# Optimization experiments

Hardware: AMD Instinct MI355X
Metric: run time of the kernel (lower is better)

## Reference

```python
import jax, jax.numpy as jnp
import numpy as np

TAKE = 64
HID = 64


def setup_inputs() -> dict:
    key = jax.random.key(0)
    ks = jax.random.split(key, 12)
    B, N, C = 32, 1000, 1601
    s = 1.0 / np.sqrt(C)
    s2 = 1.0 / np.sqrt(HID)
    return {
        "class_logits": jax.random.normal(ks[0], (B, N, C), dtype=jnp.float32),
        "proposals": jax.random.uniform(ks[1], (B, N, 4), dtype=jnp.float32),
        # subject projection (Linear stored as [in, out] so y = x @ W + b)
        "Ws1": jax.random.uniform(ks[2], (C, HID), minval=-s, maxval=s),
        "bs1": jax.random.uniform(ks[3], (HID,), minval=-s, maxval=s),
        "Ws2": jax.random.uniform(ks[4], (HID, HID), minval=-s2, maxval=s2),
        "bs2": jax.random.uniform(ks[5], (HID,), minval=-s2, maxval=s2),
        # object projection
        "Wo1": jax.random.uniform(ks[6], (C, HID), minval=-s, maxval=s),
        "bo1": jax.random.uniform(ks[7], (HID,), minval=-s, maxval=s),
        "Wo2": jax.random.uniform(ks[8], (HID, HID), minval=-s2, maxval=s2),
        "bo2": jax.random.uniform(ks[9], (HID,), minval=-s2, maxval=s2),
    }


def _mlp(x, W1, b1, W2, b2):
    # Linear -> ReLU -> Linear
    return jnp.maximum(x @ W1 + b1, 0.0) @ W2 + b2


def reference(class_logits, proposals, Ws1, bs1, Ws2, bs2, Wo1, bo1, Wo2, bo2):
    B, N, _ = class_logits.shape
    subj = _mlp(class_logits, Ws1, bs1, Ws2, bs2)  # [B, N, 64]
    obj = _mlp(class_logits, Wo1, bo1, Wo2, bo2)   # [B, N, 64]
    # relatedness[b, i, j] = sigmoid(<subj_i, obj_j>)
    scores = jax.nn.sigmoid(jnp.einsum("bnd,bmd->bnm", subj, obj))  # [B, N, N]
    flat = scores.reshape(B, N * N)
    top_scores, top_idx = jax.lax.top_k(flat, TAKE)  # descending, same as sort[:take]
    # flat index k = subject*N + object (row-major), matching the torch meshgrid
    pairs = jnp.stack([top_idx // N, top_idx % N], axis=-1)  # [B, 64, 2] (subj, obj)
    return pairs, top_scores
```

## Files before the change

kernel.cpp:

```cpp
#include <hip/hip_runtime.h>
#include <cstdint>

#define NB 32
#define NN 1000
#define NC 1601
#define HID 64
#define ROWS (NB*NN)
#define CAPB 15360
#define SROWS 15
#define NBIN 4096
#define KCH 32
#define XSTR 68
#define SSTR 132

__device__ __forceinline__ uint32_t f2key(float f){
  uint32_t u = __float_as_uint(f);
  return (u & 0x80000000u) ? ~u : (u | 0x80000000u);
}
__device__ __forceinline__ float key2f(uint32_t k){
  uint32_t u = (k & 0x80000000u) ? (k & 0x7fffffffu) : ~k;
  return __uint_as_float(u);
}

__global__ __launch_bounds__(256, 4) void mlp_kernel(
    const float* __restrict__ x,
    const float* __restrict__ Ws1, const float* __restrict__ bs1,
    const float* __restrict__ Ws2, const float* __restrict__ bs2,
    const float* __restrict__ Wo1, const float* __restrict__ bo1,
    const float* __restrict__ Wo2, const float* __restrict__ bo2,
    float* __restrict__ subj, float* __restrict__ obj)
{
  __shared__ float smem[2*KCH*XSTR];
  __shared__ float xtail[64];
  const int tid = threadIdx.x;
  const int tx  = tid & 15;
  const int ty  = tid >> 4;
  const int row0 = blockIdx.x * 64;

  float accS[4][4], accO[4][4];
  #pragma unroll
  for (int r=0;r<4;r++)
    #pragma unroll
    for (int c=0;c<4;c++){ accS[r][c]=0.f; accO[r][c]=0.f; }

  float stg[8];
  #pragma unroll
  for (int it=0; it<8; it++){
    int u = tid + it*256;
    stg[it] = x[(size_t)(row0 + (u>>5))*NC + (u&31)];
  }

  const int NCHUNK = 50;
  for (int c = 0; c < NCHUNK; c++){
    float* xT = smem + (c & 1)*(KCH*XSTR);
    #pragma unroll
    for (int it=0; it<8; it++){
      int u = tid + it*256;
      xT[(u&31)*XSTR + (u>>5)] = stg[it];
    }
    __syncthreads();
    if (c+1 < NCHUNK){
      const int k0n = (c+1)*KCH;
      #pragma unroll
      for (int it=0; it<8; it++){
        int u = tid + it*256;
        stg[it] = x[(size_t)(row0 + (u>>5))*NC + k0n + (u&31)];
      }
    }
    const float* wS = Ws1 + (size_t)(c*KCH)*HID + tx*4;
    const float* wO = Wo1 + (size_t)(c*KCH)*HID + tx*4;
    #pragma unroll 4
    for (int k=0; k<KCH; k++){
      float4 a  = *(const float4*)&xT[k*XSTR + ty*4];
      float4 bS = *(const float4*)(wS + k*HID);
      float4 bO = *(const float4*)(wO + k*HID);
      float av[4] = {a.x,a.y,a.z,a.w};
      float bs[4] = {bS.x,bS.y,bS.z,bS.w};
      float bo[4] = {bO.x,bO.y,bO.z,bO.w};
      #pragma unroll
      for (int r=0;r<4;r++)
        #pragma unroll
        for (int c2=0;c2<4;c2++){
          accS[r][c2] = fmaf(av[r], bs[c2], accS[r][c2]);
          accO[r][c2] = fmaf(av[r], bo[c2], accO[r][c2]);
        }
    }
  }

  if (tid < 64) xtail[tid] = x[(size_t)(row0 + tid)*NC + 1600];
  __syncthreads();
  {
    float4 a  = *(const float4*)&xtail[ty*4];
    float4 bS = *(const float4*)(Ws1 + (size_t)1600*HID + tx*4);
    float4 bO = *(const float4*)(Wo1 + (size_t)1600*HID + tx*4);
    float av[4] = {a.x,a.y,a.z,a.w};
    float bs[4] = {bS.x,bS.y,bS.z,bS.w};
    float bo[4] = {bO.x,bO.y,bO.z,bO.w};
    #pragma unroll
    for (int r=0;r<4;r++)
      #pragma unroll
      for (int c2=0;c2<4;c2++){
        accS[r][c2] = fmaf(av[r], bs[c2], accS[r][c2]);
        accO[r][c2] = fmaf(av[r], bo[c2], accO[r][c2]);
      }
  }

  float* hT = smem;
  #pragma unroll 1
  for (int head = 0; head < 2; head++){
    const float* b1 = head ? bo1 : bs1;
    const float* b2 = head ? bo2 : bs2;
    const float* W2 = head ? Wo2 : Ws2;
    float* yout     = head ? obj : subj;
    __syncthreads();
    #pragma unroll
    for (int jj=0; jj<4; jj++){
      float bias = b1[tx*4 + jj];
      float4 hv;
      hv.x = fmaxf((head ? accO[0][jj] : accS[0][jj]) + bias, 0.f);
      hv.y = fmaxf((head ? accO[1][jj] : accS[1][jj]) + bias, 0.f);
      hv.z = fmaxf((head ? accO[2][jj] : accS[2][jj]) + bias, 0.f);
      hv.w = fmaxf((head ? accO[3][jj] : accS[3][jj]) + bias, 0.f);
      *(float4*)&hT[(tx*4+jj)*XSTR + ty*4] = hv;
    }
    __syncthreads();
    float accY[4][4];
    #pragma unroll
    for (int c2=0;c2<4;c2++){
      float bv = b2[tx*4 + c2];
      #pragma unroll
      for (int r=0;r<4;r++) accY[r][c2] = bv;
    }
    #pragma unroll 4
    for (int d=0; d<64; d++){
      float4 a = *(const float4*)&hT[d*XSTR + ty*4];
      float4 w = *(const float4*)(W2 + d*HID + tx*4);
      float av[4] = {a.x,a.y,a.z,a.w};
      float wv[4] = {w.x,w.y,w.z,w.w};
      #pragma unroll
      for (int r=0;r<4;r++)
        #pragma unroll
        for (int c2=0;c2<4;c2++)
          accY[r][c2] = fmaf(av[r], wv[c2], accY[r][c2]);
    }
    #pragma unroll
    for (int r=0;r<4;r++)
      *(float4*)&yout[(size_t)(row0 + ty*4 + r)*HID + tx*4] =
        make_float4(accY[r][0], accY[r][1], accY[r][2], accY[r][3]);
  }
}

__global__ __launch_bounds__(256, 1) void sample_thresh(
    const float* __restrict__ subj, const float* __restrict__ obj,
    uint32_t* __restrict__ L)
{
  __shared__ float sRows[SROWS*HID];
  __shared__ uint32_t keys[SROWS*NN];
  __shared__ uint32_t hist[256];
  __shared__ uint32_t sb[2];
  const int b = blockIdx.x, tid = threadIdx.x;

  const float4* sp = (const float4*)(subj + (size_t)b*NN*HID);
  if (tid < SROWS*16) ((float4*)sRows)[tid] = sp[tid];
  __syncthreads();

  for (int j = tid; j < NN; j += 256){
    const float4* op4 = (const float4*)(obj + ((size_t)b*NN + j)*HID);
    float4 o[16];
    #pragma unroll
    for (int q=0;q<16;q++) o[q] = op4[q];
    #pragma unroll 1
    for (int i=0;i<SROWS;i++){
      const float4* s4 = (const float4*)(sRows + i*HID);
      float acc = 0.f;
      #pragma unroll
      for (int q=0;q<16;q++){
        float4 s = s4[q];
        acc = fmaf(s.x, o[q].x, acc); acc = fmaf(s.y, o[q].y, acc);
        acc = fmaf(s.z, o[q].z, acc); acc = fmaf(s.w, o[q].w, acc);
      }
      keys[i*NN + j] = f2key(acc);
    }
  }
  __syncthreads();

  uint32_t prefix = 0; int remaining = 64;
  for (int round = 0; round < 2; round++){
    const int shift = 24 - round*8;
    hist[tid] = 0;
    __syncthreads();
    for (int idx = tid; idx < SROWS*NN; idx += 256){
      uint32_t k = keys[idx];
      bool match = (round == 0) || ((k >> 24) == (prefix >> 24));
      if (match) atomicAdd(&hist[(k >> shift) & 255u], 1u);
    }
    __syncthreads();
    if (tid == 0){
      uint32_t cum = 0; int bin = 255;
      for (;; bin--){ cum += hist[bin]; if (cum >= (uint32_t)remaining || bin == 0) break; }
      sb[0] = (uint32_t)bin;
      sb[1] = (uint32_t)(remaining - (int)(cum - hist[bin]));
    }
    __syncthreads();
    prefix |= sb[0] << shift;
    remaining = (int)sb[1];
    __syncthreads();
  }
  if (tid == 0) L[b] = prefix;
}

__device__ __forceinline__ void score_tile_acc(
    const float* __restrict__ subj, const float* __restrict__ obj,
    int b, int ti, int tj, int tid,
    float* __restrict__ sT, float* __restrict__ oT, float (&acc)[8][8])
{
  const int tx = tid & 15, ty = tid >> 4;
  #pragma unroll
  for (int a=0;a<8;a++)
    #pragma unroll
    for (int c=0;c<8;c++) acc[a][c] = 0.f;

  #pragma unroll 1
  for (int half = 0; half < 2; half++){
    __syncthreads();
    {
      const float4* gp = (const float4*)subj;
      #pragma unroll
      for (int it=0; it<4; it++){
        int u = tid + it*256;
        int r = u >> 3, q = (u & 7) + half*8;
        int gr = b*NN + ti + r; gr = gr < ROWS ? gr : (ROWS-1);
        float4 v = gp[(size_t)gr*16 + q];
        int kk = (u & 7)*4;
        sT[(kk+0)*SSTR + r] = v.x;
        sT[(kk+1)*SSTR + r] = v.y;
        sT[(kk+2)*SSTR + r] = v.z;
        sT[(kk+3)*SSTR + r] = v.w;
      }
      const float4* gp2 = (const float4*)obj;
      #pragma unroll
      for (int it=0; it<4; it++){
        int u = tid + it*256;
        int r = u >> 3, q = (u & 7) + half*8;
        int gr = b*NN + tj + r; gr = gr < ROWS ? gr : (ROWS-1);
        float4 v = gp2[(size_t)gr*16 + q];
        int kk = (u & 7)*4;
        oT[(kk+0)*SSTR + r] = v.x;
        oT[(kk+1)*SSTR + r] = v.y;
        oT[(kk+2)*SSTR + r] = v.z;
        oT[(kk+3)*SSTR + r] = v.w;
      }
    }
    __syncthreads();
    #pragma unroll 2
    for (int k=0; k<32; k++){
      float4 s0 = *(const float4*)&sT[k*SSTR + ty*8];
      float4 s1 = *(const float4*)&sT[k*SSTR + ty*8 + 4];
      float4 o0 = *(const float4*)&oT[k*SSTR + tx*8];
      float4 o1 = *(const float4*)&oT[k*SSTR + tx*8 + 4];
      float s[8] = {s0.x,s0.y,s0.z,s0.w,s1.x,s1.y,s1.z,s1.w};
      float o[8] = {o0.x,o0.y,o0.z,o0.w,o1.x,o1.y,o1.z,o1.w};
      #pragma unroll
      for (int a=0;a<8;a++)
        #pragma unroll
        for (int c=0;c<8;c++)
          acc[a][c] = fmaf(s[a], o[c], acc[a][c]);
    }
  }
}

__global__ __launch_bounds__(256, 3) void score_pass1(
    const float* __restrict__ subj, const float* __restrict__ obj,
    const uint32_t* __restrict__ L, uint32_t* __restrict__ cnt,
    uint2* __restrict__ cand, uint32_t* __restrict__ ghist)
{
  __shared__ float sT[32*SSTR];
  __shared__ float oT[32*SSTR];
  __shared__ uint32_t hist[NBIN];
  __shared__ uint32_t lcnt, gbase;
  const int blk = blockIdx.x;
  const int b   = blk >> 6;
  const int t   = blk & 63;
  const int ti  = (t >> 3) << 7;
  const int tj  = (t & 7)  << 7;
  const int tid = threadIdx.x;
  const int tx = tid & 15, ty = tid >> 4;

  for (int i = tid; i < NBIN; i += 256) hist[i] = 0;
  if (tid == 0) lcnt = 0;

  float acc[8][8];
  score_tile_acc(subj, obj, b, ti, tj, tid, sT, oT, acc);

  const uint32_t Lb = L[b];
  int myCnt = 0;
  #pragma unroll
  for (int a=0;a<8;a++){
    int gi = ti + ty*8 + a;
    #pragma unroll
    for (int c=0;c<8;c++){
      int gj = tj + tx*8 + c;
      if (gi < NN && gj < NN){
        uint32_t key = f2key(acc[a][c]);
        if (key >= Lb){ myCnt++; atomicAdd(&hist[key >> 20], 1u); }
      }
    }
  }
  uint32_t lbase = atomicAdd(&lcnt, (uint32_t)myCnt);
  __syncthreads();
  if (tid == 0) gbase = atomicAdd(&cnt[b], lcnt);
  __syncthreads();
  uint32_t pos = gbase + lbase;
  #pragma unroll
  for (int a=0;a<8;a++){
    int gi = ti + ty*8 + a;
    #pragma unroll
    for (int c=0;c<8;c++){
      int gj = tj + tx*8 + c;
      if (gi < NN && gj < NN){
        uint32_t key = f2key(acc[a][c]);
        if (key >= Lb){
          if (pos < CAPB) cand[(size_t)b*CAPB + pos] = make_uint2(key, (uint32_t)(gi*NN + gj));
          pos++;
        }
      }
    }
  }
  __syncthreads();
  for (int i = tid; i < NBIN; i += 256){
    uint32_t v = hist[i];
    if (v) atomicAdd(&ghist[(size_t)b*NBIN + i], v);
  }
}

__global__ __launch_bounds__(256, 1) void pick_thresh(
    const uint32_t* __restrict__ ghist, const uint32_t* __restrict__ cnt,
    uint32_t* __restrict__ T, uint32_t* __restrict__ flag)
{
  __shared__ uint32_t S[256];
  const int b = blockIdx.x, tid = threadIdx.x;
  const uint32_t* h = ghist + (size_t)b*NBIN;
  uint32_t loc[16];
  uint32_t s = 0;
  #pragma unroll
  for (int i=0;i<16;i++){ loc[i] = h[tid*16 + i]; s += loc[i]; }
  S[tid] = s;
  __syncthreads();
  for (int off = 1; off < 256; off <<= 1){
    uint32_t v = (tid + off < 256) ? S[tid + off] : 0u;
    __syncthreads();
    S[tid] += v;
    __syncthreads();
  }
  uint32_t above = (tid < 255) ? S[tid + 1] : 0u;
  if (above < 64u && S[tid] >= 64u){
    uint32_t suf = above; int best = 0;
    for (int i=15;i>=0;i--){ suf += loc[i]; if (suf >= 64u){ best = i; break; } }
    T[b] = (uint32_t)(tid*16 + best) << 20;
  }
  if (tid == 0) flag[b] = (cnt[b] > (uint32_t)CAPB) ? 1u : 0u;
}

__global__ __launch_bounds__(256, 3) void score_repair(
    const float* __restrict__ subj, const float* __restrict__ obj,
    const uint32_t* __restrict__ T, const uint32_t* __restrict__ flag,
    uint32_t* __restrict__ cnt2, uint2* __restrict__ cand)
{
  const int blk = blockIdx.x;
  const int b   = blk >> 6;
  if (flag[b] == 0u) return;

  __shared__ float sT[32*SSTR];
  __shared__ float oT[32*SSTR];
  __shared__ uint32_t lcnt, gbase;
  const int t   = blk & 63;
  const int ti  = (t >> 3) << 7;
  const int tj  = (t & 7)  << 7;
  const int tid = threadIdx.x;
  const int tx = tid & 15, ty = tid >> 4;

  if (tid == 0) lcnt = 0;

  float acc[8][8];
  score_tile_acc(subj, obj, b, ti, tj, tid, sT, oT, acc);

  const uint32_t Tb = T[b];
  int myCnt = 0;
  #pragma unroll
  for (int a=0;a<8;a++){
    int gi = ti + ty*8 + a;
    #pragma unroll
    for (int c=0;c<8;c++){
      int gj = tj + tx*8 + c;
      if (gi < NN && gj < NN && f2key(acc[a][c]) >= Tb) myCnt++;
    }
  }
  uint32_t lbase = atomicAdd(&lcnt, (uint32_t)myCnt);
  __syncthreads();
  if (tid == 0) gbase = atomicAdd(&cnt2[b], lcnt);
  __syncthreads();
  uint32_t pos = gbase + lbase;
  #pragma unroll
  for (int a=0;a<8;a++){
    int gi = ti + ty*8 + a;
    #pragma unroll
    for (int c=0;c<8;c++){
      int gj = tj + tx*8 + c;
      if (gi < NN && gj < NN){
        uint32_t key = f2key(acc[a][c]);
        if (key >= Tb){
          if (pos < CAPB) cand[(size_t)b*CAPB + pos] = make_uint2(key, (uint32_t)(gi*NN + gj));
          pos++;
        }
      }
    }
  }
}

__global__ __launch_bounds__(256, 1) void final_select(
    const uint32_t* __restrict__ cnt, const uint32_t* __restrict__ cnt2,
    const uint32_t* __restrict__ flag, const uint2* __restrict__ cand,
    float* __restrict__ out)
{
  __shared__ uint32_t keys[CAPB];
  __shared__ uint32_t hist[256];
  __shared__ uint32_t sb[2];
  __shared__ uint2 win[192];
  __shared__ uint32_t wn;
  const int b = blockIdx.x, tid = threadIdx.x;
  uint32_t n0 = flag[b] ? cnt2[b] : cnt[b];
  const int n = (n0 < (uint32_t)CAPB) ? (int)n0 : CAPB;

  for (int i = tid; i < n; i += 256) keys[i] = cand[(size_t)b*CAPB + i].x;
  if (tid == 0) wn = 0;
  __syncthreads();

  uint32_t prefix = 0; int remaining = 64;
  for (int round = 0; round < 4; round++){
    const int shift = 24 - round*8;
    hist[tid] = 0;
    __syncthreads();
    for (int i = tid; i < n; i += 256){
      uint32_t k = keys[i];
      bool match = (round == 0) || ((k >> (shift+8)) == (prefix >> (shift+8)));
      if (match) atomicAdd(&hist[(k >> shift) & 255u], 1u);
    }
    __syncthreads();
    if (tid == 0){
      uint32_t cum = 0; int bin = 255;
      for (;; bin--){ cum += hist[bin]; if (cum >= (uint32_t)remaining || bin == 0) break; }
      sb[0] = (uint32_t)bin;
      sb[1] = (uint32_t)(remaining - (int)(cum - hist[bin]));
    }
    __syncthreads();
    prefix |= sb[0] << shift;
    remaining = (int)sb[1];
    __syncthreads();
  }
  const uint32_t Tk = prefix;

  for (int i = tid; i < n; i += 256){
    if (keys[i] >= Tk){
      uint32_t p = atomicAdd(&wn, 1u);
      if (p < 192u) win[p] = make_uint2(keys[i], cand[(size_t)b*CAPB + i].y);
    }
  }
  __syncthreads();
  const int m = (wn < 192u) ? (int)wn : 192;

  if (tid < m){
    const uint64_t me = ((uint64_t)win[tid].x << 32) | (uint64_t)(uint32_t)(~win[tid].y);
    int rank = 0;
    for (int s = 0; s < m; s++){
      uint64_t oth = ((uint64_t)win[s].x << 32) | (uint64_t)(uint32_t)(~win[s].y);
      rank += (oth > me) ? 1 : 0;
    }
    if (rank < 64){
      const uint32_t f = win[tid].y;
      const float d  = key2f(win[tid].x);
      const float sc = 1.0f / (1.0f + expf(-d));
      out[((size_t)b*64 + rank)*2 + 0] = (float)(f / NN);
      out[((size_t)b*64 + rank)*2 + 1] = (float)(f % NN);
      out[(size_t)NB*64*2 + (size_t)b*64 + rank] = sc;
    }
  }
}

extern "C" void kernel_launch(void* const* d_in, const int* in_sizes, int n_in,
                              void* d_out, int out_size, void* d_ws, size_t ws_size,
                              hipStream_t stream) {
  const float* x   = (const float*)d_in[0];
  const float* Ws1 = (const float*)d_in[2];
  const float* bs1 = (const float*)d_in[3];
  const float* Ws2 = (const float*)d_in[4];
  const float* bs2 = (const float*)d_in[5];
  const float* Wo1 = (const float*)d_in[6];
  const float* bo1 = (const float*)d_in[7];
  const float* Wo2 = (const float*)d_in[8];
  const float* bo2 = (const float*)d_in[9];
  float* out = (float*)d_out;

  char* ws = (char*)d_ws;
  float*    subj = (float*)ws;
  float*    objp = (float*)(ws + 8192000);
  uint32_t* L    = (uint32_t*)(ws + 16384000);
  uint32_t* cnt  = (uint32_t*)(ws + 16384128);
  uint32_t* cnt2 = (uint32_t*)(ws + 16384256);
  uint32_t* ghist= (uint32_t*)(ws + 16384384);
  uint32_t* T    = (uint32_t*)(ws + 16908672);
  uint32_t* flag = (uint32_t*)(ws + 16908800);
  uint2*    cand = (uint2*)   (ws + 16908928);

  hipMemsetAsync(cnt, 0, 128 + 128 + 524288, stream);

  mlp_kernel<<<ROWS/64, 256, 0, stream>>>(x, Ws1, bs1, Ws2, bs2,
                                          Wo1, bo1, Wo2, bo2, subj, objp);
  sample_thresh<<<NB, 256, 0, stream>>>(subj, objp, L);
  score_pass1<<<NB*64, 256, 0, stream>>>(subj, objp, L, cnt, cand, ghist);
  pick_thresh<<<NB, 256, 0, stream>>>(ghist, cnt, T, flag);
  score_repair<<<NB*64, 256, 0, stream>>>(subj, objp, T, flag, cnt2, cand);
  final_select<<<NB, 256, 0, stream>>>(cnt, cnt2, flag, cand, out);
}
```

Baseline: 743.1 us.

## Move MLP and score GEMMs to bf16x3 split MFMA matrix cores

Replaces the FP32 FMA GEMMs in the MLP and the pairwise score tiles with MFMA 16x16x32 bf16 instructions, splitting each fp32 value into three bf16 parts and summing six cross products to keep near-fp32 accuracy. A new prep kernel pre-splits and re-lays out the weights into bf16 planes on every call. The pass-1 threshold is loosened by a small key margin to absorb rounding differences between sampled and MFMA scores. This trades extra split work, extra shared-memory planes and lower occupancy for much higher matrix throughput.

```diff
diff --git a/kernel.cpp b/kernel.cpp
--- a/kernel.cpp
+++ b/kernel.cpp
@@ -9,9 +9,13 @@
 #define CAPB 15360
 #define SROWS 15
 #define NBIN 4096
-#define KCH 32
-#define XSTR 68
-#define SSTR 132
+#define MSTR 40
+#define HSTR 72
+#define PSTR 40
+#define PPL  (128*PSTR)
+
+typedef short short8 __attribute__((ext_vector_type(8)));
+typedef float floatx4 __attribute__((ext_vector_type(4)));
 
 __device__ __forceinline__ uint32_t f2key(float f){
   uint32_t u = __float_as_uint(f);
@@ -22,26 +26,84 @@
   return __uint_as_float(u);
 }
 
-__global__ __launch_bounds__(256, 4) void mlp_kernel(
+__device__ __forceinline__ void split3(float v, ushort& h0, ushort& h1, ushort& h2){
+  uint32_t u0 = __float_as_uint(v) & 0xffff0000u;
+  h0 = (ushort)(u0 >> 16);
+  float r1 = v - __uint_as_float(u0);
+  uint32_t u1 = __float_as_uint(r1) & 0xffff0000u;
+  h1 = (ushort)(u1 >> 16);
+  float r2 = r1 - __uint_as_float(u1);
+  h2 = (ushort)(__float_as_uint(r2) >> 16);
+}
+
+#define MFMA6(acc, A0,A1,A2, B0,B1,B2) do { \
+  acc = __builtin_amdgcn_mfma_f32_16x16x32_bf16(A0,B0,acc,0,0,0); \
+  acc = __builtin_amdgcn_mfma_f32_16x16x32_bf16(A0,B1,acc,0,0,0); \
+  acc = __builtin_amdgcn_mfma_f32_16x16x32_bf16(A1,B0,acc,0,0,0); \
+  acc = __builtin_amdgcn_mfma_f32_16x16x32_bf16(A1,B1,acc,0,0,0); \
+  acc = __builtin_amdgcn_mfma_f32_16x16x32_bf16(A2,B0,acc,0,0,0); \
+  acc = __builtin_amdgcn_mfma_f32_16x16x32_bf16(A0,B2,acc,0,0,0); } while(0)
+
+__global__ __launch_bounds__(256, 1) void prep_w(
+    const float* __restrict__ Ws1, const float* __restrict__ Wo1,
+    const float* __restrict__ Ws2, const float* __restrict__ Wo2,
+    ushort* __restrict__ w1s, ushort* __restrict__ w2s)
+{
+  int idx = blockIdx.x*256 + threadIdx.x;
+  if (idx < 2*51*2048){
+    int head = idx / (51*2048);
+    int rem  = idx % (51*2048);
+    int step = rem >> 11;
+    int n    = (rem >> 5) & 63;
+    int k    = rem & 31;
+    int kg   = step*32 + k;
+    const float* W = head ? Wo1 : Ws1;
+    float v = (kg < NC) ? W[(size_t)kg*HID + n] : 0.f;
+    ushort h0,h1,h2; split3(v,h0,h1,h2);
+    size_t base = (size_t)head*3*104448 + rem;
+    w1s[base]            = h0;
+    w1s[base + 104448]   = h1;
+    w1s[base + 2*104448] = h2;
+  } else {
+    int idx2 = idx - 2*51*2048;
+    if (idx2 < 2*4096){
+      int head = idx2 >> 12;
+      int rem  = idx2 & 4095;
+      int step = rem >> 11;
+      int n    = (rem >> 5) & 63;
+      int k    = rem & 31;
+      int kg   = step*32 + k;
+      const float* W = head ? Wo2 : Ws2;
+      float v = W[(size_t)kg*HID + n];
+      ushort h0,h1,h2; split3(v,h0,h1,h2);
+      size_t base = (size_t)head*3*4096 + rem;
+      w2s[base]          = h0;
+      w2s[base + 4096]   = h1;
+      w2s[base + 2*4096] = h2;
+    }
+  }
+}
+
+__global__ __launch_bounds__(256) void mlp_mfma(
     const float* __restrict__ x,
-    const float* __restrict__ Ws1, const float* __restrict__ bs1,
-    const float* __restrict__ Ws2, const float* __restrict__ bs2,
-    const float* __restrict__ Wo1, const float* __restrict__ bo1,
-    const float* __restrict__ Wo2, const float* __restrict__ bo2,
+    const ushort* __restrict__ w1s, const ushort* __restrict__ w2s,
+    const float* __restrict__ bs1, const float* __restrict__ bs2,
+    const float* __restrict__ bo1, const float* __restrict__ bo2,
     float* __restrict__ subj, float* __restrict__ obj)
 {
-  __shared__ float smem[2*KCH*XSTR];
-  __shared__ float xtail[64];
-  const int tid = threadIdx.x;
-  const int tx  = tid & 15;
-  const int ty  = tid >> 4;
+  __shared__ __align__(16) ushort xpl[2][3][64*MSTR];
+  const int tid  = threadIdx.x;
+  const int lane = tid & 63;
+  const int wave = tid >> 6;
+  const int col  = lane & 15;
+  const int quad = lane >> 4;
   const int row0 = blockIdx.x * 64;
 
-  float accS[4][4], accO[4][4];
-  #pragma unroll
-  for (int r=0;r<4;r++)
-    #pragma unroll
-    for (int c=0;c<4;c++){ accS[r][c]=0.f; accO[r][c]=0.f; }
+  floatx4 acc[2][4];
+  #pragma unroll
+  for (int h=0; h<2; h++)
+    #pragma unroll
+    for (int nt=0; nt<4; nt++) acc[h][nt] = (floatx4){0.f,0.f,0.f,0.f};
 
   float stg[8];
   #pragma unroll
@@ -50,103 +112,90 @@
     stg[it] = x[(size_t)(row0 + (u>>5))*NC + (u&31)];
   }
 
-  const int NCHUNK = 50;
-  for (int c = 0; c < NCHUNK; c++){
-    float* xT = smem + (c & 1)*(KCH*XSTR);
+  for (int s = 0; s < 51; s++){
+    ushort (*xb)[64*MSTR] = xpl[s & 1];
     #pragma unroll
     for (int it=0; it<8; it++){
       int u = tid + it*256;
-      xT[(u&31)*XSTR + (u>>5)] = stg[it];
-    }
-    __syncthreads();
-    if (c+1 < NCHUNK){
-      const int k0n = (c+1)*KCH;
+      int a = (u>>5)*MSTR + (u&31);
+      ushort h0,h1,h2; split3(stg[it], h0,h1,h2);
+      xb[0][a]=h0; xb[1][a]=h1; xb[2][a]=h2;
+    }
+    __syncthreads();
+    if (s+1 < 51){
       #pragma unroll
       for (int it=0; it<8; it++){
         int u = tid + it*256;
-        stg[it] = x[(size_t)(row0 + (u>>5))*NC + k0n + (u&31)];
-      }
-    }
-    const float* wS = Ws1 + (size_t)(c*KCH)*HID + tx*4;
-    const float* wO = Wo1 + (size_t)(c*KCH)*HID + tx*4;
-    #pragma unroll 4
-    for (int k=0; k<KCH; k++){
-      float4 a  = *(const float4*)&xT[k*XSTR + ty*4];
-      float4 bS = *(const float4*)(wS + k*HID);
-      float4 bO = *(const float4*)(wO + k*HID);
-      float av[4] = {a.x,a.y,a.z,a.w};
-      float bs[4] = {bS.x,bS.y,bS.z,bS.w};
-      float bo[4] = {bO.x,bO.y,bO.z,bO.w};
-      #pragma unroll
-      for (int r=0;r<4;r++)
+        int kg = (s+1)*32 + (u&31);
+        stg[it] = (kg < NC) ? x[(size_t)(row0 + (u>>5))*NC + kg] : 0.f;
+      }
+    }
+    short8 Bf[2][4][3];
+    #pragma unroll
+    for (int h=0; h<2; h++)
+      #pragma unroll
+      for (int nt=0; nt<4; nt++)
         #pragma unroll
-        for (int c2=0;c2<4;c2++){
-          accS[r][c2] = fmaf(av[r], bs[c2], accS[r][c2]);
-          accO[r][c2] = fmaf(av[r], bo[c2], accO[r][c2]);
-        }
-    }
-  }
-
-  if (tid < 64) xtail[tid] = x[(size_t)(row0 + tid)*NC + 1600];
-  __syncthreads();
-  {
-    float4 a  = *(const float4*)&xtail[ty*4];
-    float4 bS = *(const float4*)(Ws1 + (size_t)1600*HID + tx*4);
-    float4 bO = *(const float4*)(Wo1 + (size_t)1600*HID + tx*4);
-    float av[4] = {a.x,a.y,a.z,a.w};
-    float bs[4] = {bS.x,bS.y,bS.z,bS.w};
-    float bo[4] = {bO.x,bO.y,bO.z,bO.w};
-    #pragma unroll
-    for (int r=0;r<4;r++)
-      #pragma unroll
-      for (int c2=0;c2<4;c2++){
-        accS[r][c2] = fmaf(av[r], bs[c2], accS[r][c2]);
-        accO[r][c2] = fmaf(av[r], bo[c2], accO[r][c2]);
-      }
-  }
-
-  float* hT = smem;
+        for (int p=0; p<3; p++)
+          Bf[h][nt][p] = *(const short8*)(w1s +
+              (size_t)(((h*3+p)*51 + s)*2048 + nt*512 + col*32 + quad*8));
+    short8 Af[3];
+    #pragma unroll
+    for (int p=0; p<3; p++)
+      Af[p] = *(const short8*)&xb[p][(wave*16 + col)*MSTR + quad*8];
+    #pragma unroll
+    for (int h=0; h<2; h++)
+      #pragma unroll
+      for (int nt=0; nt<4; nt++)
+        MFMA6(acc[h][nt], Af[0],Af[1],Af[2], Bf[h][nt][0],Bf[h][nt][1],Bf[h][nt][2]);
+  }
+  __syncthreads();
+
+  ushort* hp = &xpl[0][0][0];
   #pragma unroll 1
-  for (int head = 0; head < 2; head++){
-    const float* b1 = head ? bo1 : bs1;
-    const float* b2 = head ? bo2 : bs2;
-    const float* W2 = head ? Wo2 : Ws2;
-    float* yout     = head ? obj : subj;
-    __syncthreads();
-    #pragma unroll
-    for (int jj=0; jj<4; jj++){
-      float bias = b1[tx*4 + jj];
-      float4 hv;
-      hv.x = fmaxf((head ? accO[0][jj] : accS[0][jj]) + bias, 0.f);
-      hv.y = fmaxf((head ? accO[1][jj] : accS[1][jj]) + bias, 0.f);
-      hv.z = fmaxf((head ? accO[2][jj] : accS[2][jj]) + bias, 0.f);
-      hv.w = fmaxf((head ? accO[3][jj] : accS[3][jj]) + bias, 0.f);
-      *(float4*)&hT[(tx*4+jj)*XSTR + ty*4] = hv;
-    }
-    __syncthreads();
-    float accY[4][4];
-    #pragma unroll
-    for (int c2=0;c2<4;c2++){
-      float bv = b2[tx*4 + c2];
-      #pragma unroll
-      for (int r=0;r<4;r++) accY[r][c2] = bv;
-    }
-    #pragma unroll 4
-    for (int d=0; d<64; d++){
-      float4 a = *(const float4*)&hT[d*XSTR + ty*4];
-      float4 w = *(const float4*)(W2 + d*HID + tx*4);
-      float av[4] = {a.x,a.y,a.z,a.w};
-      float wv[4] = {w.x,w.y,w.z,w.w};
-      #pragma unroll
-      for (int r=0;r<4;r++)
+  for (int h=0; h<2; h++){
+    const float* b1 = h ? bo1 : bs1;
+    const float* b2 = h ? bo2 : bs2;
+    float* yout = h ? obj : subj;
+    #pragma unroll
+    for (int nt=0; nt<4; nt++){
+      float bias = b1[nt*16 + col];
+      #pragma unroll
+      for (int r=0; r<4; r++){
+        float hv = fmaxf(acc[h][nt][r] + bias, 0.f);
+        ushort h0,h1,h2; split3(hv,h0,h1,h2);
+        int a = (wave*16 + quad*4 + r)*HSTR + nt*16 + col;
+        hp[a] = h0; hp[64*HSTR + a] = h1; hp[2*64*HSTR + a] = h2;
+      }
+    }
+    floatx4 acc2[4];
+    #pragma unroll
+    for (int nt=0; nt<4; nt++) acc2[nt] = (floatx4){0.f,0.f,0.f,0.f};
+    #pragma unroll
+    for (int t=0; t<2; t++){
+      short8 Af2[3];
+      #pragma unroll
+      for (int p=0; p<3; p++)
+        Af2[p] = *(const short8*)&hp[p*64*HSTR + (wave*16 + col)*HSTR + t*32 + quad*8];
+      #pragma unroll
+      for (int nt=0; nt<4; nt++){
+        short8 Bq[3];
         #pragma unroll
-        for (int c2=0;c2<4;c2++)
-          accY[r][c2] = fmaf(av[r], wv[c2], accY[r][c2]);
-    }
-    #pragma unroll
-    for (int r=0;r<4;r++)
-      *(float4*)&yout[(size_t)(row0 + ty*4 + r)*HID + tx*4] =
-        make_float4(accY[r][0], accY[r][1], accY[r][2], accY[r][3]);
+        for (int p=0; p<3; p++)
+          Bq[p] = *(const short8*)(w2s +
+              (size_t)(((h*3+p)*2 + t)*2048 + nt*512 + col*32 + quad*8));
+        MFMA6(acc2[nt], Af2[0],Af2[1],Af2[2], Bq[0],Bq[1],Bq[2]);
+      }
+    }
+    #pragma unroll
+    for (int nt=0; nt<4; nt++){
+      float bv = b2[nt*16 + col];
+      #pragma unroll
+      for (int r=0; r<4; r++){
+        int gr = row0 + wave*16 + quad*4 + r;
+        yout[(size_t)gr*HID + nt*16 + col] = acc2[nt][r] + bv;
+      }
+    }
   }
 }
 
@@ -209,73 +258,85 @@
   if (tid == 0) L[b] = prefix;
 }
 
-__device__ __forceinline__ void score_tile_acc(
+__device__ __forceinline__ void score_tile_mfma(
     const float* __restrict__ subj, const float* __restrict__ obj,
     int b, int ti, int tj, int tid,
-    float* __restrict__ sT, float* __restrict__ oT, float (&acc)[8][8])
-{
-  const int tx = tid & 15, ty = tid >> 4;
-  #pragma unroll
-  for (int a=0;a<8;a++)
-    #pragma unroll
-    for (int c=0;c<8;c++) acc[a][c] = 0.f;
+    ushort* __restrict__ apl, ushort* __restrict__ bpl,
+    floatx4 (&acc)[2][8])
+{
+  const int lane = tid & 63;
+  const int wave = tid >> 6;
+  const int col  = lane & 15;
+  const int quad = lane >> 4;
+  #pragma unroll
+  for (int mt=0; mt<2; mt++)
+    #pragma unroll
+    for (int nt=0; nt<8; nt++) acc[mt][nt] = (floatx4){0.f,0.f,0.f,0.f};
 
   #pragma unroll 1
-  for (int half = 0; half < 2; half++){
-    __syncthreads();
-    {
-      const float4* gp = (const float4*)subj;
-      #pragma unroll
-      for (int it=0; it<4; it++){
-        int u = tid + it*256;
-        int r = u >> 3, q = (u & 7) + half*8;
-        int gr = b*NN + ti + r; gr = gr < ROWS ? gr : (ROWS-1);
-        float4 v = gp[(size_t)gr*16 + q];
-        int kk = (u & 7)*4;
-        sT[(kk+0)*SSTR + r] = v.x;
-        sT[(kk+1)*SSTR + r] = v.y;
-        sT[(kk+2)*SSTR + r] = v.z;
-        sT[(kk+3)*SSTR + r] = v.w;
-      }
-      const float4* gp2 = (const float4*)obj;
-      #pragma unroll
-      for (int it=0; it<4; it++){
-        int u = tid + it*256;
-        int r = u >> 3, q = (u & 7) + half*8;
-        int gr = b*NN + tj + r; gr = gr < ROWS ? gr : (ROWS-1);
-        float4 v = gp2[(size_t)gr*16 + q];
-        int kk = (u & 7)*4;
-        oT[(kk+0)*SSTR + r] = v.x;
-        oT[(kk+1)*SSTR + r] = v.y;
-        oT[(kk+2)*SSTR + r] = v.z;
-        oT[(kk+3)*SSTR + r] = v.w;
-      }
-    }
-    __syncthreads();
-    #pragma unroll 2
-    for (int k=0; k<32; k++){
-      float4 s0 = *(const float4*)&sT[k*SSTR + ty*8];
-      float4 s1 = *(const float4*)&sT[k*SSTR + ty*8 + 4];
-      float4 o0 = *(const float4*)&oT[k*SSTR + tx*8];
-      float4 o1 = *(const float4*)&oT[k*SSTR + tx*8 + 4];
-      float s[8] = {s0.x,s0.y,s0.z,s0.w,s1.x,s1.y,s1.z,s1.w};
-      float o[8] = {o0.x,o0.y,o0.z,o0.w,o1.x,o1.y,o1.z,o1.w};
-      #pragma unroll
-      for (int a=0;a<8;a++)
-        #pragma unroll
-        for (int c=0;c<8;c++)
-          acc[a][c] = fmaf(s[a], o[c], acc[a][c]);
-    }
-  }
-}
-
-__global__ __launch_bounds__(256, 3) void score_pass1(
+  for (int half=0; half<2; half++){
+    __syncthreads();
+    #pragma unroll
+    for (int it=0; it<4; it++){
+      int u = tid + it*256;
+      int r = u >> 3, q = u & 7;
+      int gr = b*NN + ti + r; gr = gr < ROWS ? gr : (ROWS-1);
+      float4 v = ((const float4*)subj)[(size_t)gr*16 + half*8 + q];
+      ushort x0,x1,x2,y0,y1,y2,z0,z1,z2,w0,w1,w2;
+      split3(v.x,x0,x1,x2); split3(v.y,y0,y1,y2);
+      split3(v.z,z0,z1,z2); split3(v.w,w0,w1,w2);
+      int a = r*PSTR + q*4;
+      *(uint2*)&apl[0*PPL + a] = make_uint2((uint32_t)x0 | ((uint32_t)y0<<16),
+                                           (uint32_t)z0 | ((uint32_t)w0<<16));
+      *(uint2*)&apl[1*PPL + a] = make_uint2((uint32_t)x1 | ((uint32_t)y1<<16),
+                                           (uint32_t)z1 | ((uint32_t)w1<<16));
+      *(uint2*)&apl[2*PPL + a] = make_uint2((uint32_t)x2 | ((uint32_t)y2<<16),
+                                           (uint32_t)z2 | ((uint32_t)w2<<16));
+    }
+    #pragma unroll
+    for (int it=0; it<4; it++){
+      int u = tid + it*256;
+      int r = u >> 3, q = u & 7;
+      int gr = b*NN + tj + r; gr = gr < ROWS ? gr : (ROWS-1);
+      float4 v = ((const float4*)obj)[(size_t)gr*16 + half*8 + q];
+      ushort x0,x1,x2,y0,y1,y2,z0,z1,z2,w0,w1,w2;
+      split3(v.x,x0,x1,x2); split3(v.y,y0,y1,y2);
+      split3(v.z,z0,z1,z2); split3(v.w,w0,w1,w2);
+      int a = r*PSTR + q*4;
+      *(uint2*)&bpl[0*PPL + a] = make_uint2((uint32_t)x0 | ((uint32_t)y0<<16),
+                                           (uint32_t)z0 | ((uint32_t)w0<<16));
+      *(uint2*)&bpl[1*PPL + a] = make_uint2((uint32_t)x1 | ((uint32_t)y1<<16),
+                                           (uint32_t)z1 | ((uint32_t)w1<<16));
+      *(uint2*)&bpl[2*PPL + a] = make_uint2((uint32_t)x2 | ((uint32_t)y2<<16),
+                                           (uint32_t)z2 | ((uint32_t)w2<<16));
+    }
+    __syncthreads();
+    short8 Af[2][3];
+    #pragma unroll
+    for (int mt=0; mt<2; mt++)
+      #pragma unroll
+      for (int p=0; p<3; p++)
+        Af[mt][p] = *(const short8*)&apl[p*PPL + (wave*32 + mt*16 + col)*PSTR + quad*8];
+    #pragma unroll
+    for (int nt=0; nt<8; nt++){
+      short8 Bf[3];
+      #pragma unroll
+      for (int p=0; p<3; p++)
+        Bf[p] = *(const short8*)&bpl[p*PPL + (nt*16 + col)*PSTR + quad*8];
+      #pragma unroll
+      for (int mt=0; mt<2; mt++)
+        MFMA6(acc[mt][nt], Af[mt][0],Af[mt][1],Af[mt][2], Bf[0],Bf[1],Bf[2]);
+    }
+  }
+}
+
+__global__ __launch_bounds__(256, 2) void score_pass1(
     const float* __restrict__ subj, const float* __restrict__ obj,
     const uint32_t* __restrict__ L, uint32_t* __restrict__ cnt,
     uint2* __restrict__ cand, uint32_t* __restrict__ ghist)
 {
-  __shared__ float sT[32*SSTR];
-  __shared__ float oT[32*SSTR];
+  __shared__ __align__(16) ushort apl[3*PPL];
+  __shared__ __align__(16) ushort bpl[3*PPL];
   __shared__ uint32_t hist[NBIN];
   __shared__ uint32_t lcnt, gbase;
   const int blk = blockIdx.x;
@@ -284,48 +345,52 @@
   const int ti  = (t >> 3) << 7;
   const int tj  = (t & 7)  << 7;
   const int tid = threadIdx.x;
-  const int tx = tid & 15, ty = tid >> 4;
+  const int lane = tid & 63, wave = tid >> 6;
+  const int col = lane & 15, quad = lane >> 4;
 
   for (int i = tid; i < NBIN; i += 256) hist[i] = 0;
   if (tid == 0) lcnt = 0;
 
-  float acc[8][8];
-  score_tile_acc(subj, obj, b, ti, tj, tid, sT, oT, acc);
-
-  const uint32_t Lb = L[b];
+  floatx4 acc[2][8];
+  score_tile_mfma(subj, obj, b, ti, tj, tid, apl, bpl, acc);
+
+  const uint32_t Lb0 = L[b];
+  const uint32_t Lb  = (Lb0 > 65536u) ? (Lb0 - 65536u) : 0u;
   int myCnt = 0;
   #pragma unroll
-  for (int a=0;a<8;a++){
-    int gi = ti + ty*8 + a;
-    #pragma unroll
-    for (int c=0;c<8;c++){
-      int gj = tj + tx*8 + c;
-      if (gi < NN && gj < NN){
-        uint32_t key = f2key(acc[a][c]);
-        if (key >= Lb){ myCnt++; atomicAdd(&hist[key >> 20], 1u); }
-      }
-    }
-  }
+  for (int mt=0; mt<2; mt++)
+    #pragma unroll
+    for (int nt=0; nt<8; nt++)
+      #pragma unroll
+      for (int r=0; r<4; r++){
+        int gi = ti + wave*32 + mt*16 + quad*4 + r;
+        int gj = tj + nt*16 + col;
+        if (gi < NN && gj < NN){
+          uint32_t key = f2key(acc[mt][nt][r]);
+          if (key >= Lb){ myCnt++; atomicAdd(&hist[key >> 20], 1u); }
+        }
+      }
   uint32_t lbase = atomicAdd(&lcnt, (uint32_t)myCnt);
   __syncthreads();
   if (tid == 0) gbase = atomicAdd(&cnt[b], lcnt);
   __syncthreads();
   uint32_t pos = gbase + lbase;
   #pragma unroll
-  for (int a=0;a<8;a++){
-    int gi = ti + ty*8 + a;
-    #pragma unroll
-    for (int c=0;c<8;c++){
-      int gj = tj + tx*8 + c;
-      if (gi < NN && gj < NN){
-        uint32_t key = f2key(acc[a][c]);
-        if (key >= Lb){
-          if (pos < CAPB) cand[(size_t)b*CAPB + pos] = make_uint2(key, (uint32_t)(gi*NN + gj));
-          pos++;
+  for (int mt=0; mt<2; mt++)
+    #pragma unroll
+    for (int nt=0; nt<8; nt++)
+      #pragma unroll
+      for (int r=0; r<4; r++){
+        int gi = ti + wave*32 + mt*16 + quad*4 + r;
+        int gj = tj + nt*16 + col;
+        if (gi < NN && gj < NN){
+          uint32_t key = f2key(acc[mt][nt][r]);
+          if (key >= Lb){
+            if (pos < CAPB) cand[(size_t)b*CAPB + pos] = make_uint2(key, (uint32_t)(gi*NN + gj));
+            pos++;
+          }
         }
       }
-    }
-  }
   __syncthreads();
   for (int i = tid; i < NBIN; i += 256){
     uint32_t v = hist[i];
@@ -361,7 +426,7 @@
   if (tid == 0) flag[b] = (cnt[b] > (uint32_t)CAPB) ? 1u : 0u;
 }
 
-__global__ __launch_bounds__(256, 3) void score_repair(
+__global__ __launch_bounds__(256, 2) void score_repair(
     const float* __restrict__ subj, const float* __restrict__ obj,
     const uint32_t* __restrict__ T, const uint32_t* __restrict__ flag,
     uint32_t* __restrict__ cnt2, uint2* __restrict__ cand)
@@ -370,51 +435,54 @@
   const int b   = blk >> 6;
   if (flag[b] == 0u) return;
 
-  __shared__ float sT[32*SSTR];
-  __shared__ float oT[32*SSTR];
+  __shared__ __align__(16) ushort apl[3*PPL];
+  __shared__ __align__(16) ushort bpl[3*PPL];
   __shared__ uint32_t lcnt, gbase;
   const int t   = blk & 63;
   const int ti  = (t >> 3) << 7;
   const int tj  = (t & 7)  << 7;
   const int tid = threadIdx.x;
-  const int tx = tid & 15, ty = tid >> 4;
+  const int lane = tid & 63, wave = tid >> 6;
+  const int col = lane & 15, quad = lane >> 4;
 
   if (tid == 0) lcnt = 0;
 
-  float acc[8][8];
-  score_tile_acc(subj, obj, b, ti, tj, tid, sT, oT, acc);
+  floatx4 acc[2][8];
+  score_tile_mfma(subj, obj, b, ti, tj, tid, apl, bpl, acc);
 
   const uint32_t Tb = T[b];
   int myCnt = 0;
   #pragma unroll
-  for (int a=0;a<8;a++){
-    int gi = ti + ty*8 + a;
-    #pragma unroll
-    for (int c=0;c<8;c++){
-      int gj = tj + tx*8 + c;
-      if (gi < NN && gj < NN && f2key(acc[a][c]) >= Tb) myCnt++;
-    }
-  }
+  for (int mt=0; mt<2; mt++)
+    #pragma unroll
+    for (int nt=0; nt<8; nt++)
+      #pragma unroll
+      for (int r=0; r<4; r++){
+        int gi = ti + wave*32 + mt*16 + quad*4 + r;
+        int gj = tj + nt*16 + col;
+        if (gi < NN && gj < NN && f2key(acc[mt][nt][r]) >= Tb) myCnt++;
+      }
   uint32_t lbase = atomicAdd(&lcnt, (uint32_t)myCnt);
   __syncthreads();
   if (tid == 0) gbase = atomicAdd(&cnt2[b], lcnt);
   __syncthreads();
   uint32_t pos = gbase + lbase;
   #pragma unroll
-  for (int a=0;a<8;a++){
-    int gi = ti + ty*8 + a;
-    #pragma unroll
-    for (int c=0;c<8;c++){
-      int gj = tj + tx*8 + c;
-      if (gi < NN && gj < NN){
-        uint32_t key = f2key(acc[a][c]);
-        if (key >= Tb){
-          if (pos < CAPB) cand[(size_t)b*CAPB + pos] = make_uint2(key, (uint32_t)(gi*NN + gj));
-          pos++;
+  for (int mt=0; mt<2; mt++)
+    #pragma unroll
+    for (int nt=0; nt<8; nt++)
+      #pragma unroll
+      for (int r=0; r<4; r++){
+        int gi = ti + wave*32 + mt*16 + quad*4 + r;
+        int gj = tj + nt*16 + col;
+        if (gi < NN && gj < NN){
+          uint32_t key = f2key(acc[mt][nt][r]);
+          if (key >= Tb){
+            if (pos < CAPB) cand[(size_t)b*CAPB + pos] = make_uint2(key, (uint32_t)(gi*NN + gj));
+            pos++;
+          }
         }
       }
-    }
-  }
 }
 
 __global__ __launch_bounds__(256, 1) void final_select(
@@ -510,11 +578,13 @@
   uint32_t* T    = (uint32_t*)(ws + 16908672);
   uint32_t* flag = (uint32_t*)(ws + 16908800);
   uint2*    cand = (uint2*)   (ws + 16908928);
+  ushort*   w1s  = (ushort*)  (ws + 20841088);
+  ushort*   w2s  = (ushort*)  (ws + 22094464);
 
   hipMemsetAsync(cnt, 0, 128 + 128 + 524288, stream);
 
-  mlp_kernel<<<ROWS/64, 256, 0, stream>>>(x, Ws1, bs1, Ws2, bs2,
-                                          Wo1, bo1, Wo2, bo2, subj, objp);
+  prep_w<<<848, 256, 0, stream>>>(Ws1, Wo1, Ws2, Wo2, w1s, w2s);
+  mlp_mfma<<<ROWS/64, 256, 0, stream>>>(x, w1s, w2s, bs1, bs2, bo1, bo2, subj, objp);
   sample_thresh<<<NB, 256, 0, stream>>>(subj, objp, L);
   score_pass1<<<NB*64, 256, 0, stream>>>(subj, objp, L, cnt, cand, ghist);
   pick_thresh<<<NB, 256, 0, stream>>>(ghist, cnt, T, flag);
```

Result: slower. 777.7 us (+4.7%).
